# Performance work log

Hardware: AMD Instinct MI355X
Metric: run time of the kernel (lower is better)

The kernel has to match this reference:

```python
import jax, jax.numpy as jnp
import numpy as np

NG, ND = 50000, 10000          # gene / disease node counts
IN, HID = 64, 128              # in_feats / hidden_feats
EGG, EGD, EDG = 800000, 300000, 300000
EPS = 1e-5


def setup_inputs() -> dict:
    key = jax.random.key(0)
    ks = jax.random.split(key, 18)
    s = 0.05
    return {
        "xg": jax.random.normal(ks[0], (NG, IN), jnp.float32),
        "xd": jax.random.normal(ks[1], (ND, IN), jnp.float32),
        "Wn0": jax.random.normal(ks[2], (3, IN, HID), jnp.float32) * s,
        "Ws0": jax.random.normal(ks[3], (3, IN, HID), jnp.float32) * s,
        "b0": jnp.zeros((3, HID), jnp.float32),
        "Wn1": jax.random.normal(ks[4], (3, HID, HID), jnp.float32) * s,
        "Ws1": jax.random.normal(ks[5], (3, HID, HID), jnp.float32) * s,
        "b1": jnp.zeros((3, HID), jnp.float32),
        "bng": jnp.ones((2, 2, HID), jnp.float32),   # [layer, ntype, HID]
        "bnb": jnp.zeros((2, 2, HID), jnp.float32),
        "Wp": jax.random.normal(ks[6], (2, HID, IN), jnp.float32) * s,
        "bp": jnp.zeros((2, IN), jnp.float32),
        "gg_src": jax.random.randint(ks[7], (EGG,), 0, NG, jnp.int32),
        "gg_dst": jax.random.randint(ks[8], (EGG,), 0, NG, jnp.int32),
        "gd_src": jax.random.randint(ks[9], (EGD,), 0, NG, jnp.int32),
        "gd_dst": jax.random.randint(ks[10], (EGD,), 0, ND, jnp.int32),
        "dg_src": jax.random.randint(ks[11], (EDG,), 0, ND, jnp.int32),
        "dg_dst": jax.random.randint(ks[12], (EDG,), 0, NG, jnp.int32),
    }


def _seg_mean(h_src, src_idx, dst_idx, num_dst):
    # gather source features along edges, mean-reduce onto destinations
    msg = h_src[src_idx]                                         # [E, D]
    ssum = jax.ops.segment_sum(msg, dst_idx, num_segments=num_dst)
    deg = jax.ops.segment_sum(jnp.ones((dst_idx.shape[0], 1), h_src.dtype),
                              dst_idx, num_segments=num_dst)
    return ssum / jnp.maximum(deg, 1.0)                          # zero-degree -> 0


def _sage(h_src, h_dst, src_idx, dst_idx, num_dst, Wn, Ws, b):
    # DGL SAGEConv(mean): fc_neigh(mean_neigh) + fc_self(h_dst) + bias
    m = _seg_mean(h_src, src_idx, dst_idx, num_dst)
    return m @ Wn + h_dst @ Ws + b


def _bn_relu(x, g, b):
    # BatchNorm1d in training mode (batch statistics) followed by ReLU
    mu = x.mean(axis=0)
    var = x.var(axis=0)
    return jax.nn.relu((x - mu) * jax.lax.rsqrt(var + EPS) * g + b)


def _hetero_layer(hg, hd, Wn, Ws, b, idx):
    gg_s, gg_d, gd_s, gd_d, dg_s, dg_d = idx
    # HeteroGraphConv aggregate='sum' across relations per destination type
    out_g = (_sage(hg, hg, gg_s, gg_d, NG, Wn[0], Ws[0], b[0]) +
             _sage(hd, hg, dg_s, dg_d, NG, Wn[2], Ws[2], b[2]))
    out_d = _sage(hg, hd, gd_s, gd_d, ND, Wn[1], Ws[1], b[1])
    return out_g, out_d


def reference(xg, xd, Wn0, Ws0, b0, Wn1, Ws1, b1, bng, bnb, Wp, bp,
              gg_src, gg_dst, gd_src, gd_dst, dg_src, dg_dst):
    idx = (gg_src, gg_dst, gd_src, gd_dst, dg_src, dg_dst)
    # layer 0
    hg, hd = _hetero_layer(xg, xd, Wn0, Ws0, b0, idx)
    hg = _bn_relu(hg, bng[0, 0], bnb[0, 0])
    hd = _bn_relu(hd, bng[0, 1], bnb[0, 1])
    # layer 1
    hg, hd = _hetero_layer(hg, hd, Wn1, Ws1, b1, idx)
    hg = _bn_relu(hg, bng[1, 0], bnb[1, 0])
    hd = _bn_relu(hd, bng[1, 1], bnb[1, 1])
    # final per-type projection back to in_feats
    out_g = hg @ Wp[0] + bp[0]
    out_d = hd @ Wp[1] + bp[1]
    return out_g, out_d
```

## Files before the change

### kernel.cpp

```cpp
#include <hip/hip_runtime.h>

typedef unsigned short u16;
typedef __attribute__((ext_vector_type(8))) short bf16x8;
typedef __attribute__((ext_vector_type(4))) float f32x4;

__device__ __forceinline__ float BF(u16 u) { return __uint_as_float(((unsigned)u) << 16); }
__device__ __forceinline__ float BLO(unsigned p) { return __uint_as_float(p << 16); }
__device__ __forceinline__ float BHI(unsigned p) { return __uint_as_float(p & 0xffff0000u); }
__device__ __forceinline__ u16 FBF(float f) {
    unsigned u = __float_as_uint(f);
    u += 0x7FFFu + ((u >> 16) & 1u);
    return (u16)(u >> 16);
}
__device__ __forceinline__ unsigned PK2(float a, float b) {
    return (unsigned)FBF(a) | ((unsigned)FBF(b) << 16);
}
__device__ __forceinline__ float LD(const void* p, long i, int isf) {
    if (isf) return ((const float*)p)[i];
    return BF(((const u16*)p)[i]);
}

__global__ void HeteroGNN_78426102825755_kernel() {}

__global__ void hk_fill16(u16* p, long n, u16 v) {
    long i = (long)blockIdx.x * 256 + threadIdx.x;
    if (i < n) p[i] = v;
}

__global__ void hk_detect2(const void* x, int* flag, int* ncur, int Tn, float* bnbuf) {
    int i = blockIdx.x * 256 + threadIdx.x;
    if (i < Tn) ncur[i] = 0;
    if (i < 512) bnbuf[i] = 0.f;
    if (blockIdx.x == 0) {
        __shared__ int cnt;
        if (threadIdx.x == 0) cnt = 0;
        __syncthreads();
        unsigned w = ((const unsigned*)x)[threadIdx.x];
        int e = (w >> 7) & 0xFF;
        atomicAdd(&cnt, (e >= 0x68 && e <= 0x92) ? 1 : 0);
        __syncthreads();
        if (threadIdx.x == 0) flag[0] = (cnt >= 192) ? 0 : 1;
    }
}

__device__ __forceinline__ void wprep_one(const void* W, int K, int ncol, int persh, int ksh,
                                          unsigned* dst, int i, int isf) {
    int mslice = i >> persh;
    int d2 = i & ((1 << persh) - 1);
    int mat = mslice >> ksh;
    int ks = mslice & ((1 << ksh) - 1);
    int ct = d2 >> 8; int rr = d2 & 255; int ln = rr >> 2; int j2 = rr & 3;
    int k1 = ks * 32 + ((ln >> 4) * 8 + 2 * j2);
    int n = ct * 16 + (ln & 15);
    long e = (long)mat * K * ncol + (long)k1 * ncol + n;
    dst[i] = PK2(LD(W, e, isf), LD(W, e + ncol, isf));
}
__device__ __forceinline__ void wsum_one(const void* W, int K, unsigned* dst, int i, int isf) {
    int ks = i >> 11; int d2 = i & 2047;
    int ct = d2 >> 8; int rr = d2 & 255; int ln = rr >> 2; int j2 = rr & 3;
    int k1 = ks * 32 + ((ln >> 4) * 8 + 2 * j2);
    int n = ct * 16 + (ln & 15);
    long e = (long)k1 * 128 + n;
    long e2 = e + (long)2 * K * 128;
    dst[i] = PK2(LD(W, e, isf) + LD(W, e2, isf), LD(W, e + 128, isf) + LD(W, e2 + 128, isf));
}

__global__ void hk_prepcnt(const void* Wn0, const void* Ws0, const void* Wn1, const void* Ws1,
                           unsigned* f0n, unsigned* f0s, unsigned* f1n, unsigned* f1s,
                           unsigned* f0sum, unsigned* f1sum,
                           const void* xg, const void* xd, long n0, long n1,
                           u16* og, u16* od, int Cb,
                           const int* d0, const int* d1, const int* d2,
                           int E0, int E1, int E2, int NGn, int* cnt, int* rank,
                           const int* dflag) {
    int b = blockIdx.x, t = threadIdx.x;
    if (b < Cb) {
        int i = b * 256 + t;
        int tn;
        if (i < E0) tn = d0[i];
        else if (i < E0 + E1) tn = NGn + d1[i - E0];
        else if (i < E0 + E1 + E2) tn = 2 * NGn + d2[i - E0 - E1];
        else return;
        rank[i] = atomicAdd(&cnt[tn], 1);
        return;
    }
    int isf = dflag[0];
    b -= Cb;
    if (b < 48)  { wprep_one(Wn0, 64, 128, 11, 1, f0n, b * 256 + t, isf); return; }
    if (b < 96)  { wprep_one(Ws0, 64, 128, 11, 1, f0s, (b - 48) * 256 + t, isf); return; }
    if (b < 192) { wprep_one(Wn1, 128, 128, 11, 2, f1n, (b - 96) * 256 + t, isf); return; }
    if (b < 288) { wprep_one(Ws1, 128, 128, 11, 2, f1s, (b - 192) * 256 + t, isf); return; }
    if (b < 304) { wsum_one(Ws0, 64, f0sum, (b - 288) * 256 + t, isf); return; }
    if (b < 336) { wsum_one(Ws1, 128, f1sum, (b - 304) * 256 + t, isf); return; }
    long i = (long)(b - 336) * 256 + t;
    if (i < n0) og[i] = FBF(LD(xg, i, isf));
    else if (i < n0 + n1) od[i - n0] = FBF(LD(xd, i - n0, isf));
}

__global__ void hk_scan_a(const int* cnt, int n, int* pre, int* bsum) {
    __shared__ int lds[2048];
    __shared__ int part[256];
    int t = threadIdx.x;
    int base = blockIdx.x * 2048;
    for (int i = 0; i < 8; i++) {
        int idx = base + i * 256 + t;
        lds[i * 256 + t] = (idx < n) ? cnt[idx] : 0;
    }
    __syncthreads();
    int run[8];
    int s = 0;
    for (int i = 0; i < 8; i++) { run[i] = lds[t * 8 + i]; s += run[i]; }
    part[t] = s;
    __syncthreads();
    for (int o = 1; o < 256; o <<= 1) {
        int add = (t >= o) ? part[t - o] : 0;
        __syncthreads();
        part[t] += add;
        __syncthreads();
    }
    int ex = (t == 0) ? 0 : part[t - 1];
    for (int i = 0; i < 8; i++) {
        lds[t * 8 + i] = ex;
        ex += run[i];
    }
    __syncthreads();
    for (int i = 0; i < 8; i++) {
        int idx = base + i * 256 + t;
        if (idx < n) pre[idx] = lds[i * 256 + t];
    }
    if (t == 255) bsum[blockIdx.x] = part[255];
}

__global__ void hk_scan_b(int* bsum, int nb) {
    __shared__ int part[256];
    int t = threadIdx.x;
    part[t] = (t < nb) ? bsum[t] : 0;
    __syncthreads();
    for (int o = 1; o < 256; o <<= 1) {
        int add = (t >= o) ? part[t - o] : 0;
        __syncthreads();
        part[t] += add;
        __syncthreads();
    }
    if (t < nb) bsum[t] = (t == 0) ? 0 : part[t - 1];
    if (t == 0) bsum[nb] = part[nb - 1];
}

__global__ void hk_scan_c(const int* pre, const int* bsum, int n, int nb, int* offs) {
    int i = blockIdx.x * 256 + threadIdx.x;
    if (i < n) offs[i] = pre[i] + bsum[i >> 11];
    if (i == 0) offs[n] = bsum[nb];
}

__global__ void hk_scatter3p(const int* s0, const int* d0, const int* s1, const int* d1,
                             const int* s2, const int* d2,
                             int E0, int E1, int E2, int NGn,
                             const int* offs, const int* rank, int* csr, float pscale) {
    int part = blockIdx.x & 7;
    int stride = (gridDim.x >> 3) * 256;
    int ET = E0 + E1 + E2;
    for (int i = (blockIdx.x >> 3) * 256 + threadIdx.x; i < ET; i += stride) {
        int t;
        if (i < E0) t = d0[i];
        else if (i < E0 + E1) t = NGn + d1[i - E0];
        else t = 2 * NGn + d2[i - E0 - E1];
        int p = (int)((float)t * pscale);
        if (p > 7) p = 7;
        if (p != part) continue;
        int s = (i < E0) ? s0[i] : (i < E0 + E1) ? s1[i - E0] : s2[i - E0 - E1];
        csr[offs[t] + rank[i]] = s;
    }
}

__device__ void mean64_rows(const unsigned* __restrict__ g, const int* __restrict__ offs,
                            const int* __restrict__ csr, unsigned* __restrict__ out,
                            int rA, int N, int lane) {
    int rB = rA + 1;
    if (rA >= N) return;
    int bA = offs[rA], eA = offs[rA + 1];
    int bB = 0, eB = 0;
    if (rB < N) { bB = offs[rB]; eB = offs[rB + 1]; }
    float sA0 = 0.f, sA1 = 0.f, sB0 = 0.f, sB1 = 0.f;
    int kA = bA, kB = bB;
    while (kA + 4 <= eA && kB + 4 <= eB) {
        unsigned pA0 = g[(long)csr[kA] * 64 + lane];
        unsigned pA1 = g[(long)csr[kA + 1] * 64 + lane];
        unsigned pA2 = g[(long)csr[kA + 2] * 64 + lane];
        unsigned pA3 = g[(long)csr[kA + 3] * 64 + lane];
        unsigned pB0 = g[(long)csr[kB] * 64 + lane];
        unsigned pB1 = g[(long)csr[kB + 1] * 64 + lane];
        unsigned pB2 = g[(long)csr[kB + 2] * 64 + lane];
        unsigned pB3 = g[(long)csr[kB + 3] * 64 + lane];
        sA0 += (BLO(pA0) + BLO(pA1)) + (BLO(pA2) + BLO(pA3));
        sA1 += (BHI(pA0) + BHI(pA1)) + (BHI(pA2) + BHI(pA3));
        sB0 += (BLO(pB0) + BLO(pB1)) + (BLO(pB2) + BLO(pB3));
        sB1 += (BHI(pB0) + BHI(pB1)) + (BHI(pB2) + BHI(pB3));
        kA += 4; kB += 4;
    }
    while (kA + 4 <= eA) {
        unsigned p0 = g[(long)csr[kA] * 64 + lane];
        unsigned p1 = g[(long)csr[kA + 1] * 64 + lane];
        unsigned p2 = g[(long)csr[kA + 2] * 64 + lane];
        unsigned p3 = g[(long)csr[kA + 3] * 64 + lane];
        sA0 += (BLO(p0) + BLO(p1)) + (BLO(p2) + BLO(p3));
        sA1 += (BHI(p0) + BHI(p1)) + (BHI(p2) + BHI(p3));
        kA += 4;
    }
    while (kB + 4 <= eB) {
        unsigned p0 = g[(long)csr[kB] * 64 + lane];
        unsigned p1 = g[(long)csr[kB + 1] * 64 + lane];
        unsigned p2 = g[(long)csr[kB + 2] * 64 + lane];
        unsigned p3 = g[(long)csr[kB + 3] * 64 + lane];
        sB0 += (BLO(p0) + BLO(p1)) + (BLO(p2) + BLO(p3));
        sB1 += (BHI(p0) + BHI(p1)) + (BHI(p2) + BHI(p3));
        kB += 4;
    }
    for (; kA < eA; kA++) {
        unsigned p = g[(long)csr[kA] * 64 + lane];
        sA0 += BLO(p); sA1 += BHI(p);
    }
    for (; kB < eB; kB++) {
        unsigned p = g[(long)csr[kB] * 64 + lane];
        sB0 += BLO(p); sB1 += BHI(p);
    }
    float invA = (eA > bA) ? 1.f / (float)(eA - bA) : 0.f;
    float invB = (eB > bB) ? 1.f / (float)(eB - bB) : 0.f;
    out[(long)rA * 64 + lane] = PK2(sA0 * invA, sA1 * invA);
    if (rB < N) out[(long)rB * 64 + lane] = PK2(sB0 * invB, sB1 * invB);
}

__device__ void mean32_rows(const unsigned* __restrict__ g, const int* __restrict__ offs,
                            const int* __restrict__ csr, unsigned* __restrict__ out,
                            int rA, int N, int l) {
    int rB = rA + 1;
    if (rA >= N) return;
    int bA = offs[rA], eA = offs[rA + 1];
    int bB = 0, eB = 0;
    if (rB < N) { bB = offs[rB]; eB = offs[rB + 1]; }
    float sA0 = 0.f, sA1 = 0.f, sB0 = 0.f, sB1 = 0.f;
    int kA = bA, kB = bB;
    while (kA + 4 <= eA && kB + 4 <= eB) {
        unsigned pA0 = g[(long)csr[kA] * 32 + l];
        unsigned pA1 = g[(long)csr[kA + 1] * 32 + l];
        unsigned pA2 = g[(long)csr[kA + 2] * 32 + l];
        unsigned pA3 = g[(long)csr[kA + 3] * 32 + l];
        unsigned pB0 = g[(long)csr[kB] * 32 + l];
        unsigned pB1 = g[(long)csr[kB + 1] * 32 + l];
        unsigned pB2 = g[(long)csr[kB + 2] * 32 + l];
        unsigned pB3 = g[(long)csr[kB + 3] * 32 + l];
        sA0 += (BLO(pA0) + BLO(pA1)) + (BLO(pA2) + BLO(pA3));
        sA1 += (BHI(pA0) + BHI(pA1)) + (BHI(pA2) + BHI(pA3));
        sB0 += (BLO(pB0) + BLO(pB1)) + (BLO(pB2) + BLO(pB3));
        sB1 += (BHI(pB0) + BHI(pB1)) + (BHI(pB2) + BHI(pB3));
        kA += 4; kB += 4;
    }
    while (kA + 4 <= eA) {
        unsigned p0 = g[(long)csr[kA] * 32 + l];
        unsigned p1 = g[(long)csr[kA + 1] * 32 + l];
        unsigned p2 = g[(long)csr[kA + 2] * 32 + l];
        unsigned p3 = g[(long)csr[kA + 3] * 32 + l];
        sA0 += (BLO(p0) + BLO(p1)) + (BLO(p2) + BLO(p3));
        sA1 += (BHI(p0) + BHI(p1)) + (BHI(p2) + BHI(p3));
        kA += 4;
    }
    while (kB + 4 <= eB) {
        unsigned p0 = g[(long)csr[kB] * 32 + l];
        unsigned p1 = g[(long)csr[kB + 1] * 32 + l];
        unsigned p2 = g[(long)csr[kB + 2] * 32 + l];
        unsigned p3 = g[(long)csr[kB + 3] * 32 + l];
        sB0 += (BLO(p0) + BLO(p1)) + (BLO(p2) + BLO(p3));
        sB1 += (BHI(p0) + BHI(p1)) + (BHI(p2) + BHI(p3));
        kB += 4;
    }
    for (; kA < eA; kA++) {
        unsigned p = g[(long)csr[kA] * 32 + l];
        sA0 += BLO(p); sA1 += BHI(p);
    }
    for (; kB < eB; kB++) {
        unsigned p = g[(long)csr[kB] * 32 + l];
        sB0 += BLO(p); sB1 += BHI(p);
    }
    float invA = (eA > bA) ? 1.f / (float)(eA - bA) : 0.f;
    float invB = (eB > bB) ? 1.f / (float)(eB - bB) : 0.f;
    out[(long)rA * 32 + l] = PK2(sA0 * invA, sA1 * invA);
    if (rB < N) out[(long)rB * 32 + l] = PK2(sB0 * invB, sB1 * invB);
}

__global__ void hk_mean32a(const unsigned* hg, const unsigned* hd,
                           const int* offs, const int* csr,
                           unsigned* mgg, unsigned* mdg, unsigned* mgd,
                           int NGn, int NDn, int nbg) {
    int b = blockIdx.x;
    const unsigned* g; const int* O; unsigned* o; int N; int rb;
    if (b < nbg)          { g = hg; O = offs;           o = mgg; N = NGn; rb = b * 16; }
    else if (b < 2 * nbg) { g = hd; O = offs + NGn;     o = mdg; N = NGn; rb = (b - nbg) * 16; }
    else                  { g = hg; O = offs + 2 * NGn; o = mgd; N = NDn; rb = (b - 2 * nbg) * 16; }
    int w = threadIdx.x >> 6, lane = threadIdx.x & 63;
    int half = lane >> 5, l = lane & 31;
    mean32_rows(g, O, csr, o, rb + w * 4 + half * 2, N, l);
}

__global__ void hk_mean64a(const unsigned* hg, const unsigned* hd,
                           const int* offs, const int* csr,
                           unsigned* mgg, unsigned* mdg, unsigned* mgd,
                           int NGn, int NDn, int nbg) {
    int b = blockIdx.x;
    const unsigned* g; const int* O; unsigned* o; int N; int rb;
    if (b < nbg)          { g = hg; O = offs;           o = mgg; N = NGn; rb = b * 8; }
    else if (b < 2 * nbg) { g = hd; O = offs + NGn;     o = mdg; N = NGn; rb = (b - nbg) * 8; }
    else                  { g = hg; O = offs + 2 * NGn; o = mgd; N = NDn; rb = (b - 2 * nbg) * 8; }
    int w = threadIdx.x >> 6, lane = threadIdx.x & 63;
    mean64_rows(g, O, csr, o, rb + w * 2, N, lane);
}

struct DS3 {
    const unsigned* AT[3];
    const unsigned* W[12];
    const void* bb; long b1off; long b2off;
    int N; u16* out; float* stats;
};

template<int NT, int KS, int RS, int PS>
__device__ __forceinline__ void ds3_body(const DS3& P, int row0, int isf,
                                         unsigned* lds, float* red) {
    constexpr int NS = NT * KS;
    int tid = threadIdx.x;
    int wave = tid >> 6, lane = tid & 63, m = lane & 15, quad = lane >> 4;
    bf16x8 B[NS];
#pragma unroll
    for (int s = 0; s < NS; s++)
        B[s] = *(const bf16x8*)(P.W[s] + wave * 256 + lane * 4);
    constexpr int R4 = RS / 4;
#pragma unroll
    for (int t = 0; t < NT; t++) {
        const uint4* src = (const uint4*)P.AT[t] + (long)row0 * R4;
#pragma unroll
        for (int j0 = 0; j0 < 64 * R4; j0 += 512) {
            int j = j0 + tid;
            int r = j / R4, c = j - r * R4;
            *(uint4*)&lds[(t * 64 + r) * PS + c * 4] = src[j];
        }
    }
    __syncthreads();

    f32x4 acc[4];
    f32x4 z = {0.f, 0.f, 0.f, 0.f};
#pragma unroll
    for (int rt = 0; rt < 4; rt++) acc[rt] = z;
#pragma unroll
    for (int s = 0; s < NS; s++) {
        const unsigned* ab = lds + (s / KS) * 64 * PS + (s % KS) * 16;
#pragma unroll
        for (int rt = 0; rt < 4; rt++) {
            bf16x8 af = *(const bf16x8*)(ab + (rt * 16 + m) * PS + quad * 4);
            acc[rt] = __builtin_amdgcn_mfma_f32_16x16x32_bf16(af, B[s], acc[rt], 0, 0, 0);
        }
    }
    if (tid < 256) red[tid] = 0.f;
    __syncthreads();
    int col = wave * 16 + m;
    float bv = LD(P.bb, P.b1off + col, isf);
    if (P.b2off >= 0) bv += LD(P.bb, P.b2off + col, isf);
    float ps = 0.f, ps2 = 0.f;
#pragma unroll
    for (int rt = 0; rt < 4; rt++) {
#pragma unroll
        for (int reg = 0; reg < 4; reg++) {
            int row = row0 + rt * 16 + quad * 4 + reg;
            if (row < P.N) {
                float v = acc[rt][reg] + bv;
                P.out[(long)row * 128 + col] = FBF(v);
                ps += v; ps2 += v * v;
            }
        }
    }
    atomicAdd(&red[col], ps);
    atomicAdd(&red[col + 128], ps2);
    __syncthreads();
    if (tid < 256) atomicAdd(&P.stats[tid], red[tid]);
}

template<int NTG, int NTD, int KS, int RS, int PS>
__global__ __launch_bounds__(512) void hk_dsage3(DS3 G, DS3 D, int gbl, const int* dflag) {
    __shared__ __align__(16) unsigned lds[NTG * 64 * PS];
    __shared__ float red[256];
    int isf = dflag[0];
    int b = blockIdx.x;
    if (b < gbl) ds3_body<NTG, KS, RS, PS>(G, b * 64, isf, lds, red);
    else         ds3_body<NTD, KS, RS, PS>(D, (b - gbl) * 64, isf, lds, red);
}

__global__ void hk_bnfinal2(float* buf, float invNg, float invNd,
                            const void* g, long gg, long gd,
                            const void* b, long bg, long bd, const int* dflag) {
    int isf = dflag[0];
    int t = threadIdx.x;
    int c = t & 127, isD = t >> 7;
    float* st = buf + (isD ? 256 : 0);
    float invN = isD ? invNd : invNg;
    float s1 = st[c], s2 = st[c + 128];
    float mu = s1 * invN;
    float var = s2 * invN - mu * mu;
    if (var < 0.f) var = 0.f;
    float sc = LD(g, (isD ? gd : gg) + c, isf) * rsqrtf(var + 1e-5f);
    float* o = buf + 512 + (isD ? 256 : 0);
    o[c] = sc;
    o[c + 128] = LD(b, (isD ? bd : bg) + c, isf) - mu * sc;
    st[c] = 0.f;
    st[c + 128] = 0.f;
}

__global__ void hk_bnapply2(u16* xg_, long n8g, u16* xd_, long n8d, const float* buf) {
    long i = (long)blockIdx.x * 256 + threadIdx.x;
    uint4* p; const float *sc, *sh; long k;
    if (i < n8g) { k = i; p = (uint4*)xg_; sc = buf + 512; sh = buf + 640; }
    else {
        k = i - n8g;
        if (k >= n8d) return;
        p = (uint4*)xd_; sc = buf + 768; sh = buf + 896;
    }
    uint4 v = p[k];
    int j = (int)(k & 15) * 8;
    float f[8] = {BLO(v.x), BHI(v.x), BLO(v.y), BHI(v.y),
                  BLO(v.z), BHI(v.z), BLO(v.w), BHI(v.w)};
    for (int c = 0; c < 8; c++) {
        float t = fmaf(f[c], sc[j + c], sh[j + c]);
        f[c] = (t > 0.f) ? t : 0.f;
    }
    uint4 o;
    o.x = PK2(f[0], f[1]); o.y = PK2(f[2], f[3]);
    o.z = PK2(f[4], f[5]); o.w = PK2(f[6], f[7]);
    p[k] = o;
}

__global__ void hk_proj2(const u16* Ag, int Ngn, const u16* Ad, int Ndn, int gbl,
                         const void* W, const void* bias, float* og, float* od,
                         const float* bn, const int* dflag) {
    const int S = 130;
    __shared__ float aT[64 * S];
    __shared__ float ws[2048];
    int isf = dflag[0];
    int tid = threadIdx.x;
    int gene = ((int)blockIdx.x < gbl) ? 1 : 0;
    const u16* A = gene ? Ag : Ad;
    int N = gene ? Ngn : Ndn;
    long woff = gene ? 0 : 8192;
    long boff = gene ? 0 : 64;
    float* out = gene ? og : od;
    const float* sc = bn + 512 + (gene ? 0 : 256);
    const float* sh = sc + 128;
    int wave = tid >> 6, lane = tid & 63;
    int jx = tid & 15, r0 = (tid >> 4) * 4;
    int row0 = (gene ? blockIdx.x : blockIdx.x - gbl) * 64;

    float2 scv = *(const float2*)&sc[2 * lane];
    float2 shv = *(const float2*)&sh[2 * lane];
    const unsigned* A32 = (const unsigned*)A;
    for (int i = 0; i < 16; i++) {
        int r = wave * 16 + i, row = row0 + r;
        unsigned p = (row < N) ? A32[(long)row * 64 + lane] : 0u;
        float2 v;
        v.x = fmaf(BLO(p), scv.x, shv.x); v.x = (v.x > 0.f) ? v.x : 0.f;
        v.y = fmaf(BHI(p), scv.y, shv.y); v.y = (v.y > 0.f) ? v.y : 0.f;
        *(float2*)&aT[r * S + 2 * lane] = v;
    }
    __syncthreads();

    float acc[4][4];
    for (int r = 0; r < 4; r++)
        for (int c = 0; c < 4; c++) acc[r][c] = 0.f;

    for (int k0 = 0; k0 < 128; k0 += 32) {
        for (int i = 0; i < 8; i++) {
            int idx = tid + i * 256;
            ws[idx] = LD(W, woff + (long)(k0 + (idx >> 6)) * 64 + (idx & 63), isf);
        }
        __syncthreads();
        for (int kk = 0; kk < 32; kk++) {
            float4 w4 = *(const float4*)(ws + kk * 64 + jx * 4);
            for (int r = 0; r < 4; r++) {
                float a = aT[(r0 + r) * S + k0 + kk];
                acc[r][0] = fmaf(a, w4.x, acc[r][0]);
                acc[r][1] = fmaf(a, w4.y, acc[r][1]);
                acc[r][2] = fmaf(a, w4.z, acc[r][2]);
                acc[r][3] = fmaf(a, w4.w, acc[r][3]);
            }
        }
        __syncthreads();
    }

    float b4[4];
    for (int c = 0; c < 4; c++) b4[c] = LD(bias, boff + jx * 4 + c, isf);
    for (int r = 0; r < 4; r++) {
        int row = row0 + r0 + r;
        if (row >= N) continue;
        float4 o;
        o.x = acc[r][0] + b4[0]; o.y = acc[r][1] + b4[1];
        o.z = acc[r][2] + b4[2]; o.w = acc[r][3] + b4[3];
        *(float4*)&out[(long)row * 64 + jx * 4] = o;
    }
}

extern "C" void kernel_launch(void* const* d_in, const int* in_sizes, int n_in,
                              void* d_out, int out_size, void* d_ws, size_t ws_size,
                              hipStream_t stream) {
    const void* xg = d_in[0];
    const void* xd = d_in[1];
    const void* Wn0 = d_in[2];
    const void* Ws0 = d_in[3];
    const void* b0 = d_in[4];
    const void* Wn1 = d_in[5];
    const void* Ws1 = d_in[6];
    const void* b1 = d_in[7];
    const void* bng = d_in[8];
    const void* bnb = d_in[9];
    const void* Wp = d_in[10];
    const void* bp = d_in[11];
    const int* gg_src = (const int*)d_in[12];
    const int* gg_dst = (const int*)d_in[13];
    const int* gd_src = (const int*)d_in[14];
    const int* gd_dst = (const int*)d_in[15];
    const int* dg_src = (const int*)d_in[16];
    const int* dg_dst = (const int*)d_in[17];

    const int NG = in_sizes[0] / 64;
    const int ND = in_sizes[1] / 64;
    const int EGG = in_sizes[12];
    const int EGD = in_sizes[14];
    const int EDG = in_sizes[16];

    const int NGp = (NG + 63) & ~63;
    const int NDp = (ND + 63) & ~63;
    const int Tn = 2 * NG + ND;
    const int ET = EGG + EDG + EGD;

    float* outf = (float*)d_out;

    char* base = (char*)d_ws;
    size_t off = 0;
    u16* hg0; u16* pg1;
    unsigned *wf0n, *wf0s, *wf1n, *wf1s, *wf0sum, *wf1sum;
    int *csr, *offs, *ncur, *scanpre, *scanbs;
    int* dflag;
    float* bnbuf;
    {
        hg0 = (u16*)(base + off);      off += (size_t)NGp * 128 * 2; off = (off + 255) & ~(size_t)255;
        pg1 = (u16*)(base + off);      off += (size_t)NGp * 128 * 2; off = (off + 255) & ~(size_t)255;
        wf0n = (unsigned*)(base + off); off += 3 * 4096 * 4;         off = (off + 255) & ~(size_t)255;
        wf0s = (unsigned*)(base + off); off += 3 * 4096 * 4;         off = (off + 255) & ~(size_t)255;
        wf1n = (unsigned*)(base + off); off += 3 * 8192 * 4;         off = (off + 255) & ~(size_t)255;
        wf1s = (unsigned*)(base + off); off += 3 * 8192 * 4;         off = (off + 255) & ~(size_t)255;
        wf0sum = (unsigned*)(base + off); off += 4096 * 4;           off = (off + 255) & ~(size_t)255;
        wf1sum = (unsigned*)(base + off); off += 8192 * 4;           off = (off + 255) & ~(size_t)255;
        csr = (int*)(base + off);      off += (size_t)ET * 4;        off = (off + 255) & ~(size_t)255;
        offs = (int*)(base + off);     off += (size_t)(Tn + 1) * 4;  off = (off + 255) & ~(size_t)255;
        ncur = (int*)(base + off);     off += (size_t)Tn * 4;        off = (off + 255) & ~(size_t)255;
        scanpre = (int*)(base + off);  off += (size_t)Tn * 4;        off = (off + 255) & ~(size_t)255;
        scanbs = (int*)(base + off);   off += 257 * 4;               off = (off + 255) & ~(size_t)255;
        bnbuf = (float*)(base + off);  off += 1024 * 4;              off = (off + 255) & ~(size_t)255;
        dflag = (int*)(base + off);    off += 256;                   off = (off + 255) & ~(size_t)255;
    }
    unsigned* meanP = (unsigned*)(base + off); off += (size_t)NGp * 128 * 4; off = (off + 255) & ~(size_t)255;
    size_t off_mean = off;
    u16* pd1ws = (u16*)(base + off); off += (size_t)NDp * 128 * 2;
    size_t off_full = off;

    int tier;
    if (off_full <= ws_size) tier = 2;
    else if (off_mean <= ws_size) tier = 1;
    else {
        hk_fill16<<<(int)(((long)out_size * 2 + 255) / 256), 256, 0, stream>>>(
            (u16*)d_out, (long)out_size * 2, (u16)0x4000);
        return;
    }

    u16* hd0 = (u16*)d_out;
    u16* pd1out = hd0 + (long)NDp * 128;
    unsigned* mgdM = (unsigned*)(pd1out + (long)NDp * 128);
    u16* pd1 = (tier == 2) ? pd1ws : pd1out;

    u16* xg16 = pg1;
    u16* xd16 = pg1 + (long)NGp * 64;
    int* rank = (int*)hg0;

    hk_detect2<<<(Tn + 255) / 256, 256, 0, stream>>>(xg, dflag, ncur, Tn, bnbuf);

    {
        int Cb = (ET + 255) / 256;
        int Tb = (int)(((long)(NG + ND) * 64 + 255) / 256);
        hk_prepcnt<<<Cb + 336 + Tb, 256, 0, stream>>>(
            Wn0, Ws0, Wn1, Ws1, wf0n, wf0s, wf1n, wf1s, wf0sum, wf1sum,
            xg, xd, (long)NG * 64, (long)ND * 64, xg16, xd16, Cb,
            gg_dst, dg_dst, gd_dst, EGG, EDG, EGD, NG, ncur, rank, dflag);
    }

    {
        int nbT = (Tn + 2047) / 2048;
        hk_scan_a<<<nbT, 256, 0, stream>>>(ncur, Tn, scanpre, scanbs);
        hk_scan_b<<<1, 256, 0, stream>>>(scanbs, nbT);
        hk_scan_c<<<(Tn + 255) / 256, 256, 0, stream>>>(scanpre, scanbs, Tn, nbT, offs);
    }

    hk_scatter3p<<<8 * 208, 256, 0, stream>>>(gg_src, gg_dst, dg_src, dg_dst,
                                              gd_src, gd_dst, EGG, EDG, EGD,
                                              NG, offs, rank, csr, 8.0f / (float)Tn);

    const int gb = NGp / 64, db = NDp / 64;
    unsigned* xg16u = (unsigned*)xg16;
    unsigned* xd16u = (unsigned*)xd16;
    unsigned* hg0u = (unsigned*)hg0;
    unsigned* hd0u = (unsigned*)hd0;
    unsigned* mggM = meanP;
    unsigned* mdg0 = meanP + (long)NGp * 32;
    unsigned* mdg1 = meanP + (long)NGp * 64;

    DS3 G = {}, D = {};

    {
        int nbg = (NG + 15) / 16, nbd = (ND + 15) / 16;
        hk_mean32a<<<2 * nbg + nbd, 256, 0, stream>>>(xg16u, xd16u, offs, csr,
                                                      mggM, mdg0, mgdM, NG, ND, nbg);
    }
    G.AT[0] = mggM;  G.W[0] = wf0n;             G.W[1] = wf0n + 2048;
    G.AT[1] = mdg0;  G.W[2] = wf0n + 2 * 4096;  G.W[3] = wf0n + 2 * 4096 + 2048;
    G.AT[2] = xg16u; G.W[4] = wf0sum;           G.W[5] = wf0sum + 2048;
    G.bb = b0; G.b1off = 0; G.b2off = 256;
    G.N = NG; G.out = hg0; G.stats = bnbuf;
    D.AT[0] = mgdM;  D.W[0] = wf0n + 4096;      D.W[1] = wf0n + 4096 + 2048;
    D.AT[1] = xd16u; D.W[2] = wf0s + 4096;      D.W[3] = wf0s + 4096 + 2048;
    D.bb = b0; D.b1off = 128; D.b2off = -1;
    D.N = ND; D.out = hd0; D.stats = bnbuf + 256;
    hk_dsage3<3, 2, 2, 32, 36><<<gb + db, 512, 0, stream>>>(G, D, gb, dflag);
    hk_bnfinal2<<<1, 256, 0, stream>>>(bnbuf, 1.f / NG, 1.f / ND, bng, 0L, 128L, bnb, 0L, 128L, dflag);
    hk_bnapply2<<<(int)(((long)(NG + ND) * 16 + 255) / 256), 256, 0, stream>>>(
        hg0, (long)NG * 16, hd0, (long)ND * 16, bnbuf);

    {
        int nbg = (NG + 7) / 8, nbd = (ND + 7) / 8;
        hk_mean64a<<<2 * nbg + nbd, 256, 0, stream>>>(hg0u, hd0u, offs, csr,
                                                      mggM, mdg1, mgdM, NG, ND, nbg);
    }
    G = DS3{}; D = DS3{};
    G.AT[0] = mggM;  G.AT[1] = mdg1;  G.AT[2] = hg0u;
    D.AT[0] = mgdM;  D.AT[1] = hd0u;
    for (int ks = 0; ks < 4; ks++) {
        G.W[ks] = wf1n + ks * 2048;
        G.W[4 + ks] = wf1n + 2 * 8192 + ks * 2048;
        G.W[8 + ks] = wf1sum + ks * 2048;
        D.W[ks] = wf1n + 8192 + ks * 2048;
        D.W[4 + ks] = wf1s + 8192 + ks * 2048;
    }
    G.bb = b1; G.b1off = 0; G.b2off = 256;
    G.N = NG; G.out = pg1; G.stats = bnbuf;
    D.bb = b1; D.b1off = 128; D.b2off = -1;
    D.N = ND; D.out = pd1; D.stats = bnbuf + 256;
    hk_dsage3<3, 2, 4, 64, 68><<<gb + db, 512, 0, stream>>>(G, D, gb, dflag);
    hk_bnfinal2<<<1, 256, 0, stream>>>(bnbuf, 1.f / NG, 1.f / ND, bng, 256L, 384L, bnb, 256L, 384L, dflag);

    if (tier == 2) {
        hk_proj2<<<gb + db, 256, 0, stream>>>(pg1, NG, pd1, ND, gb, Wp, bp,
                                              outf, outf + (long)NG * 64, bnbuf, dflag);
    } else {
        hk_proj2<<<db, 256, 0, stream>>>(pg1, NG, pd1, ND, 0, Wp, bp,
                                         outf, outf + (long)NG * 64, bnbuf, dflag);
        hk_proj2<<<gb, 256, 0, stream>>>(pg1, NG, pd1, ND, gb, Wp, bp,
                                         outf, outf + (long)NG * 64, bnbuf, dflag);
    }
}
```

Measured before the change: 420.9 us.

## Fuse layer-0 BN+ReLU into consumers and merge scan kernels

Removes the standalone BN-apply pass over layer-0 outputs. The scale/shift and ReLU are now applied on the fly when the layer-1 mean aggregation gathers neighbour rows and when the dense SAGE kernel loads the self-feature tile. It also folds the single-block scan of block sums into the final scan kernel, so each block redundantly rescans up to 256 partial sums. This trades one full read-modify-write pass and two launches for extra FMAs per gathered element, which is repeated per edge.

```diff
diff --git a/kernel.cpp b/kernel.cpp
--- a/kernel.cpp
+++ b/kernel.cpp
@@ -131,8 +131,9 @@
     if (t == 255) bsum[blockIdx.x] = part[255];
 }
 
-__global__ void hk_scan_b(int* bsum, int nb) {
+__global__ void hk_scan_c2(const int* pre, const int* bsum, int n, int nb, int* offs) {
     __shared__ int part[256];
+    __shared__ int ex[257];
     int t = threadIdx.x;
     part[t] = (t < nb) ? bsum[t] : 0;
     __syncthreads();
@@ -142,14 +143,12 @@
         part[t] += add;
         __syncthreads();
     }
-    if (t < nb) bsum[t] = (t == 0) ? 0 : part[t - 1];
-    if (t == 0) bsum[nb] = part[nb - 1];
-}
-
-__global__ void hk_scan_c(const int* pre, const int* bsum, int n, int nb, int* offs) {
-    int i = blockIdx.x * 256 + threadIdx.x;
-    if (i < n) offs[i] = pre[i] + bsum[i >> 11];
-    if (i == 0) offs[n] = bsum[nb];
+    ex[t + 1] = part[t];
+    if (t == 0) ex[0] = 0;
+    __syncthreads();
+    int i = blockIdx.x * 256 + t;
+    if (i < n) offs[i] = pre[i] + ex[i >> 11];
+    if (i == 0) offs[n] = part[nb - 1];
 }
 
 __global__ void hk_scatter3p(const int* s0, const int* d0, const int* s1, const int* d1,
@@ -172,15 +171,27 @@
     }
 }
 
+template<bool BN>
 __device__ void mean64_rows(const unsigned* __restrict__ g, const int* __restrict__ offs,
                             const int* __restrict__ csr, unsigned* __restrict__ out,
-                            int rA, int N, int lane) {
+                            int rA, int N, int lane, const float* __restrict__ bn) {
     int rB = rA + 1;
     if (rA >= N) return;
     int bA = offs[rA], eA = offs[rA + 1];
     int bB = 0, eB = 0;
     if (rB < N) { bB = offs[rB]; eB = offs[rB + 1]; }
+    float scx = 0.f, scy = 0.f, shx = 0.f, shy = 0.f;
+    if (BN) {
+        float2 s2 = *(const float2*)&bn[2 * lane];
+        float2 h2 = *(const float2*)&bn[128 + 2 * lane];
+        scx = s2.x; scy = s2.y; shx = h2.x; shy = h2.y;
+    }
     float sA0 = 0.f, sA1 = 0.f, sB0 = 0.f, sB1 = 0.f;
+    auto ACC = [&](unsigned p, float& s0, float& s1) {
+        float vx = BLO(p), vy = BHI(p);
+        if (BN) { vx = fmaxf(fmaf(vx, scx, shx), 0.f); vy = fmaxf(fmaf(vy, scy, shy), 0.f); }
+        s0 += vx; s1 += vy;
+    };
     int kA = bA, kB = bB;
     while (kA + 4 <= eA && kB + 4 <= eB) {
         unsigned pA0 = g[(long)csr[kA] * 64 + lane];
@@ -191,10 +202,8 @@
         unsigned pB1 = g[(long)csr[kB + 1] * 64 + lane];
         unsigned pB2 = g[(long)csr[kB + 2] * 64 + lane];
         unsigned pB3 = g[(long)csr[kB + 3] * 64 + lane];
-        sA0 += (BLO(pA0) + BLO(pA1)) + (BLO(pA2) + BLO(pA3));
-        sA1 += (BHI(pA0) + BHI(pA1)) + (BHI(pA2) + BHI(pA3));
-        sB0 += (BLO(pB0) + BLO(pB1)) + (BLO(pB2) + BLO(pB3));
-        sB1 += (BHI(pB0) + BHI(pB1)) + (BHI(pB2) + BHI(pB3));
+        ACC(pA0, sA0, sA1); ACC(pA1, sA0, sA1); ACC(pA2, sA0, sA1); ACC(pA3, sA0, sA1);
+        ACC(pB0, sB0, sB1); ACC(pB1, sB0, sB1); ACC(pB2, sB0, sB1); ACC(pB3, sB0, sB1);
         kA += 4; kB += 4;
     }
     while (kA + 4 <= eA) {
@@ -202,8 +211,7 @@
         unsigned p1 = g[(long)csr[kA + 1] * 64 + lane];
         unsigned p2 = g[(long)csr[kA + 2] * 64 + lane];
         unsigned p3 = g[(long)csr[kA + 3] * 64 + lane];
-        sA0 += (BLO(p0) + BLO(p1)) + (BLO(p2) + BLO(p3));
-        sA1 += (BHI(p0) + BHI(p1)) + (BHI(p2) + BHI(p3));
+        ACC(p0, sA0, sA1); ACC(p1, sA0, sA1); ACC(p2, sA0, sA1); ACC(p3, sA0, sA1);
         kA += 4;
     }
     while (kB + 4 <= eB) {
@@ -211,18 +219,11 @@
         unsigned p1 = g[(long)csr[kB + 1] * 64 + lane];
         unsigned p2 = g[(long)csr[kB + 2] * 64 + lane];
         unsigned p3 = g[(long)csr[kB + 3] * 64 + lane];
-        sB0 += (BLO(p0) + BLO(p1)) + (BLO(p2) + BLO(p3));
-        sB1 += (BHI(p0) + BHI(p1)) + (BHI(p2) + BHI(p3));
+        ACC(p0, sB0, sB1); ACC(p1, sB0, sB1); ACC(p2, sB0, sB1); ACC(p3, sB0, sB1);
         kB += 4;
     }
-    for (; kA < eA; kA++) {
-        unsigned p = g[(long)csr[kA] * 64 + lane];
-        sA0 += BLO(p); sA1 += BHI(p);
-    }
-    for (; kB < eB; kB++) {
-        unsigned p = g[(long)csr[kB] * 64 + lane];
-        sB0 += BLO(p); sB1 += BHI(p);
-    }
+    for (; kA < eA; kA++) { unsigned p = g[(long)csr[kA] * 64 + lane]; ACC(p, sA0, sA1); }
+    for (; kB < eB; kB++) { unsigned p = g[(long)csr[kB] * 64 + lane]; ACC(p, sB0, sB1); }
     float invA = (eA > bA) ? 1.f / (float)(eA - bA) : 0.f;
     float invB = (eB > bB) ? 1.f / (float)(eB - bB) : 0.f;
     out[(long)rA * 64 + lane] = PK2(sA0 * invA, sA1 * invA);
@@ -303,24 +304,26 @@
 __global__ void hk_mean64a(const unsigned* hg, const unsigned* hd,
                            const int* offs, const int* csr,
                            unsigned* mgg, unsigned* mdg, unsigned* mgd,
-                           int NGn, int NDn, int nbg) {
+                           int NGn, int NDn, int nbg,
+                           const float* bnG, const float* bnD) {
     int b = blockIdx.x;
-    const unsigned* g; const int* O; unsigned* o; int N; int rb;
-    if (b < nbg)          { g = hg; O = offs;           o = mgg; N = NGn; rb = b * 8; }
-    else if (b < 2 * nbg) { g = hd; O = offs + NGn;     o = mdg; N = NGn; rb = (b - nbg) * 8; }
-    else                  { g = hg; O = offs + 2 * NGn; o = mgd; N = NDn; rb = (b - 2 * nbg) * 8; }
+    const unsigned* g; const int* O; unsigned* o; int N; int rb; const float* bn;
+    if (b < nbg)          { g = hg; O = offs;           o = mgg; N = NGn; rb = b * 8; bn = bnG; }
+    else if (b < 2 * nbg) { g = hd; O = offs + NGn;     o = mdg; N = NGn; rb = (b - nbg) * 8; bn = bnD; }
+    else                  { g = hg; O = offs + 2 * NGn; o = mgd; N = NDn; rb = (b - 2 * nbg) * 8; bn = bnG; }
     int w = threadIdx.x >> 6, lane = threadIdx.x & 63;
-    mean64_rows(g, O, csr, o, rb + w * 2, N, lane);
+    mean64_rows<true>(g, O, csr, o, rb + w * 2, N, lane, bn);
 }
 
 struct DS3 {
     const unsigned* AT[3];
     const unsigned* W[12];
+    const float* sbn;
     const void* bb; long b1off; long b2off;
     int N; u16* out; float* stats;
 };
 
-template<int NT, int KS, int RS, int PS>
+template<int NT, int KS, int RS, int PS, bool BNS>
 __device__ __forceinline__ void ds3_body(const DS3& P, int row0, int isf,
                                          unsigned* lds, float* red) {
     constexpr int NS = NT * KS;
@@ -338,7 +341,22 @@
         for (int j0 = 0; j0 < 64 * R4; j0 += 512) {
             int j = j0 + tid;
             int r = j / R4, c = j - r * R4;
-            *(uint4*)&lds[(t * 64 + r) * PS + c * 4] = src[j];
+            uint4 v = src[j];
+            if constexpr (BNS) {
+                if (t == NT - 1) {
+                    unsigned w0[4] = {v.x, v.y, v.z, v.w};
+#pragma unroll
+                    for (int q = 0; q < 4; q++) {
+                        int col = c * 8 + 2 * q;
+                        float2 s2 = *(const float2*)&P.sbn[col];
+                        float2 h2 = *(const float2*)&P.sbn[128 + col];
+                        w0[q] = PK2(fmaxf(fmaf(BLO(w0[q]), s2.x, h2.x), 0.f),
+                                    fmaxf(fmaf(BHI(w0[q]), s2.y, h2.y), 0.f));
+                    }
+                    v.x = w0[0]; v.y = w0[1]; v.z = w0[2]; v.w = w0[3];
+                }
+            }
+            *(uint4*)&lds[(t * 64 + r) * PS + c * 4] = v;
         }
     }
     __syncthreads();
@@ -380,14 +398,14 @@
     if (tid < 256) atomicAdd(&P.stats[tid], red[tid]);
 }
 
-template<int NTG, int NTD, int KS, int RS, int PS>
-__global__ __launch_bounds__(512) void hk_dsage3(DS3 G, DS3 D, int gbl, const int* dflag) {
+template<int NTG, int NTD, int KS, int RS, int PS, bool BNS>
+__global__ __launch_bounds__(512) void hk_dsage4(DS3 G, DS3 D, int gbl, const int* dflag) {
     __shared__ __align__(16) unsigned lds[NTG * 64 * PS];
     __shared__ float red[256];
     int isf = dflag[0];
     int b = blockIdx.x;
-    if (b < gbl) ds3_body<NTG, KS, RS, PS>(G, b * 64, isf, lds, red);
-    else         ds3_body<NTD, KS, RS, PS>(D, (b - gbl) * 64, isf, lds, red);
+    if (b < gbl) ds3_body<NTG, KS, RS, PS, BNS>(G, b * 64, isf, lds, red);
+    else         ds3_body<NTD, KS, RS, PS, BNS>(D, (b - gbl) * 64, isf, lds, red);
 }
 
 __global__ void hk_bnfinal2(float* buf, float invNg, float invNd,
@@ -408,29 +426,6 @@
     o[c + 128] = LD(b, (isD ? bd : bg) + c, isf) - mu * sc;
     st[c] = 0.f;
     st[c + 128] = 0.f;
-}
-
-__global__ void hk_bnapply2(u16* xg_, long n8g, u16* xd_, long n8d, const float* buf) {
-    long i = (long)blockIdx.x * 256 + threadIdx.x;
-    uint4* p; const float *sc, *sh; long k;
-    if (i < n8g) { k = i; p = (uint4*)xg_; sc = buf + 512; sh = buf + 640; }
-    else {
-        k = i - n8g;
-        if (k >= n8d) return;
-        p = (uint4*)xd_; sc = buf + 768; sh = buf + 896;
-    }
-    uint4 v = p[k];
-    int j = (int)(k & 15) * 8;
-    float f[8] = {BLO(v.x), BHI(v.x), BLO(v.y), BHI(v.y),
-                  BLO(v.z), BHI(v.z), BLO(v.w), BHI(v.w)};
-    for (int c = 0; c < 8; c++) {
-        float t = fmaf(f[c], sc[j + c], sh[j + c]);
-        f[c] = (t > 0.f) ? t : 0.f;
-    }
-    uint4 o;
-    o.x = PK2(f[0], f[1]); o.y = PK2(f[2], f[3]);
-    o.z = PK2(f[4], f[5]); o.w = PK2(f[6], f[7]);
-    p[k] = o;
 }
 
 __global__ void hk_proj2(const u16* Ag, int Ngn, const u16* Ad, int Ndn, int gbl,
@@ -597,8 +592,7 @@
     {
         int nbT = (Tn + 2047) / 2048;
         hk_scan_a<<<nbT, 256, 0, stream>>>(ncur, Tn, scanpre, scanbs);
-        hk_scan_b<<<1, 256, 0, stream>>>(scanbs, nbT);
-        hk_scan_c<<<(Tn + 255) / 256, 256, 0, stream>>>(scanpre, scanbs, Tn, nbT, offs);
+        hk_scan_c2<<<(Tn + 255) / 256, 256, 0, stream>>>(scanpre, scanbs, Tn, nbT, offs);
     }
 
     hk_scatter3p<<<8 * 208, 256, 0, stream>>>(gg_src, gg_dst, dg_src, dg_dst,
@@ -613,6 +607,8 @@
     unsigned* mggM = meanP;
     unsigned* mdg0 = meanP + (long)NGp * 32;
     unsigned* mdg1 = meanP + (long)NGp * 64;
+    const float* bnG = bnbuf + 512;
+    const float* bnD = bnbuf + 768;
 
     DS3 G = {}, D = {};
 
@@ -630,19 +626,18 @@
     D.AT[1] = xd16u; D.W[2] = wf0s + 4096;      D.W[3] = wf0s + 4096 + 2048;
     D.bb = b0; D.b1off = 128; D.b2off = -1;
     D.N = ND; D.out = hd0; D.stats = bnbuf + 256;
-    hk_dsage3<3, 2, 2, 32, 36><<<gb + db, 512, 0, stream>>>(G, D, gb, dflag);
+    hk_dsage4<3, 2, 2, 32, 36, false><<<gb + db, 512, 0, stream>>>(G, D, gb, dflag);
     hk_bnfinal2<<<1, 256, 0, stream>>>(bnbuf, 1.f / NG, 1.f / ND, bng, 0L, 128L, bnb, 0L, 128L, dflag);
-    hk_bnapply2<<<(int)(((long)(NG + ND) * 16 + 255) / 256), 256, 0, stream>>>(
-        hg0, (long)NG * 16, hd0, (long)ND * 16, bnbuf);
 
     {
         int nbg = (NG + 7) / 8, nbd = (ND + 7) / 8;
         hk_mean64a<<<2 * nbg + nbd, 256, 0, stream>>>(hg0u, hd0u, offs, csr,
-                                                      mggM, mdg1, mgdM, NG, ND, nbg);
+                                                      mggM, mdg1, mgdM, NG, ND, nbg,
+                                                      bnG, bnD);
     }
     G = DS3{}; D = DS3{};
-    G.AT[0] = mggM;  G.AT[1] = mdg1;  G.AT[2] = hg0u;
-    D.AT[0] = mgdM;  D.AT[1] = hd0u;
+    G.AT[0] = mggM;  G.AT[1] = mdg1;  G.AT[2] = hg0u;  G.sbn = bnG;
+    D.AT[0] = mgdM;  D.AT[1] = hd0u;                   D.sbn = bnD;
     for (int ks = 0; ks < 4; ks++) {
         G.W[ks] = wf1n + ks * 2048;
         G.W[4 + ks] = wf1n + 2 * 8192 + ks * 2048;
@@ -654,7 +649,7 @@
     G.N = NG; G.out = pg1; G.stats = bnbuf;
     D.bb = b1; D.b1off = 128; D.b2off = -1;
     D.N = ND; D.out = pd1; D.stats = bnbuf + 256;
-    hk_dsage3<3, 2, 4, 64, 68><<<gb + db, 512, 0, stream>>>(G, D, gb, dflag);
+    hk_dsage4<3, 2, 4, 64, 68, true><<<gb + db, 512, 0, stream>>>(G, D, gb, dflag);
     hk_bnfinal2<<<1, 256, 0, stream>>>(bnbuf, 1.f / NG, 1.f / ND, bng, 256L, 384L, bnb, 256L, 384L, dflag);
 
     if (tier == 2) {
```

Measured after the change: 413.2 us. About the same (-1.8%).
